# Kernel optimization log

Hardware: AMD Instinct MI355X
Metric: run time of the kernel (lower is better)

Reference implementation:

```python
import math
import jax, jax.numpy as jnp
import numpy as np

N_HEADS = 32
N_KV_HEADS = 8
HEAD_DIM = 64
DIM = 2048
SEQ = 4096
EST_Q = 64          # idx = min(64, seqlen)
VERTICAL_SIZE = 300 # min(prompt_len, max(300, 30))
SLASH_SIZE = 800    # min(prompt_len, max(800, 50))


def apply_rope(t, cos, sin):
    # t: [B,S,H,hd]; pairs are consecutive (reshape(...,-1,2) in torch view_as_complex)
    B, S, H, hd = t.shape
    tr = t.reshape(B, S, H, hd // 2, 2)
    xr, xi = tr[..., 0], tr[..., 1]
    c = cos[None, :, None, :]
    s = sin[None, :, None, :]
    orr = xr * c - xi * s
    oii = xr * s + xi * c
    return jnp.stack([orr, oii], axis=-1).reshape(B, S, H, hd)


def sum_all_diagonal(mat):
    # faithful jax version of torch as_strided trick: sum over anti-shifted diagonals
    # mat: [b,h,n,m] -> [b,h,n+m-1]; sum_diags[j] = sum_i mat[i, i + j - n], j in [1, n+m-1]
    b, h, n, m = mat.shape
    padded = jnp.pad(mat, ((0, 0), (0, 0), (0, 0), (n, n)))
    gidx = jnp.arange(n)[:, None] + jnp.arange(n + m)[None, :]  # [n, n+m]
    diags = jnp.take_along_axis(padded, jnp.broadcast_to(gidx, (b, h, n, n + m)), axis=-1)
    return diags.sum(axis=2)[:, :, 1:]


def setup_inputs() -> dict:
    key = jax.random.key(0)
    ks = jax.random.split(key, 6)
    x = jax.random.normal(ks[0], (1, SEQ, DIM), dtype=jnp.float32)
    # real RoPE tables (theta = 10000)
    inv_freq = 1.0 / (10000.0 ** (np.arange(0, HEAD_DIM, 2, dtype=np.float32) / HEAD_DIM))
    ang = np.outer(np.arange(SEQ, dtype=np.float32), inv_freq)  # [S, hd/2]
    freqs_cos = jnp.asarray(np.cos(ang), dtype=jnp.float32)
    freqs_sin = jnp.asarray(np.sin(ang), dtype=jnp.float32)
    scale = 0.02
    wq = jax.random.normal(ks[1], (DIM, N_HEADS * HEAD_DIM), dtype=jnp.float32) * scale
    wk = jax.random.normal(ks[2], (DIM, N_KV_HEADS * HEAD_DIM), dtype=jnp.float32) * scale
    wv = jax.random.normal(ks[3], (DIM, N_KV_HEADS * HEAD_DIM), dtype=jnp.float32) * scale
    wo = jax.random.normal(ks[4], (N_HEADS * HEAD_DIM, DIM), dtype=jnp.float32) * scale
    return {"x": x, "freqs_cos": freqs_cos, "freqs_sin": freqs_sin,
            "wq": wq, "wk": wk, "wv": wv, "wo": wo}


def reference(x, freqs_cos, freqs_sin, wq, wk, wv, wo):
    B, S, D = x.shape
    H, Hkv, hd = N_HEADS, N_KV_HEADS, HEAD_DIM
    rep = H // Hkv
    scale = 1.0 / math.sqrt(hd)

    # QKV + RoPE (K gets RoPE, V does not), GQA repeat
    q = apply_rope((x @ wq).reshape(B, S, H, hd), freqs_cos, freqs_sin).transpose(0, 2, 1, 3)
    k = apply_rope((x @ wk).reshape(B, S, Hkv, hd), freqs_cos, freqs_sin)
    v = (x @ wv).reshape(B, S, Hkv, hd)
    k = jnp.repeat(k, rep, axis=2).transpose(0, 2, 1, 3)  # [B,H,S,hd]
    v = jnp.repeat(v, rep, axis=2).transpose(0, 2, 1, 3)

    # --- vertical / slash pattern estimation (first idx queries, as in source) ---
    idx = min(EST_Q, S)
    qe = q[:, :, :idx, :]
    est = jnp.einsum('bhqd,bhkd->bhqk', qe, k) * scale  # [B,H,idx,S]
    ar = jnp.arange(idx)
    blk = ar[:, None] >= ar[None, :]
    tail = jnp.where(blk[None, None], est[..., -idx:], -jnp.inf)
    est = jnp.concatenate([est[..., :S - idx], tail], axis=-1)
    probs = jax.nn.softmax(est, axis=-1)

    Vn = min(S, VERTICAL_SIZE)
    Sl = min(S, SLASH_SIZE)
    vertical = probs.sum(axis=2)                  # [B,H,S]
    _, v_idx = jax.lax.top_k(vertical, Vn)        # [B,H,Vn]
    diag = sum_all_diagonal(probs)[..., :S]       # [..., :-idx+1] -> length S
    _, s_idx = jax.lax.top_k(diag, Sl)
    slash = S - 1 - s_idx                         # [B,H,Sl]

    sparse_keys = jnp.sort(jnp.concatenate([v_idx, slash], axis=-1), axis=-1)  # [B,H,K]

    # --- sparse causal attention over selected keys ---
    k_sp = jnp.take_along_axis(k, sparse_keys[..., None], axis=2)  # [B,H,K,hd]
    v_sp = jnp.take_along_axis(v, sparse_keys[..., None], axis=2)
    att = jnp.einsum('bhqd,bhkd->bhqk', q, k_sp) * scale           # [B,H,S,K]
    causal = sparse_keys[:, :, None, :] <= jnp.arange(S)[None, None, :, None]
    att = jnp.where(causal, att, -1e30)
    p = jax.nn.softmax(att, axis=-1)
    out = jnp.einsum('bhqk,bhkd->bhqd', p, v_sp)
    out = out.transpose(0, 2, 1, 3).reshape(B, S, H * hd)
    return out @ wo
```

## Files before the change

### kernel.cpp

```cpp
#include <hip/hip_runtime.h>
#include <hip/hip_bf16.h>
#include <math.h>
#include <stdint.h>

#define SEQ   4096
#define DIMM  2048
#define NH    32
#define NKV   8
#define HD    64
#define NSP   1100
#define NSPP  1152

typedef __bf16 bf16x8 __attribute__((ext_vector_type(8)));
typedef float  f32x4  __attribute__((ext_vector_type(4)));

#define MODE_V 0
#define MODE_Q 1
#define MODE_O 2

__device__ inline void split8(const float* __restrict__ p, bf16x8& h, bf16x8& l) {
#pragma unroll
    for (int i = 0; i < 8; ++i) {
        float v = p[i];
        __bf16 hv = (__bf16)v;
        h[i] = hv;
        l[i] = (__bf16)(v - (float)hv);
    }
}
__device__ inline f32x4 load4(const void* __restrict__ p, size_t idx, bool f) {
    if (f) return *(const f32x4*)((const float*)p + idx);
    const __bf16* b = (const __bf16*)p + idx;
    f32x4 v;
    v[0] = (float)b[0]; v[1] = (float)b[1]; v[2] = (float)b[2]; v[3] = (float)b[3];
    return v;
}
__device__ __forceinline__ void gl_lds16(const __bf16* __restrict__ g, __bf16* l) {
    __builtin_amdgcn_global_load_lds(
        (const __attribute__((address_space(1))) void*)g,
        (__attribute__((address_space(3))) void*)l, 16, 0, 0);
}
__device__ __forceinline__ void cs_at(const void* fc, const void* fs, bool f,
                                      int t, int j, float& c, float& s) {
    if (f) {
        c = ((const float*)fc)[t * 32 + j];
        s = ((const float*)fs)[t * 32 + j];
    } else {
        c = (float)((const __bf16*)fc)[t * 32 + j];
        s = (float)((const __bf16*)fs)[t * 32 + j];
    }
}

__global__ __launch_bounds__(256) void detect_k(const void* __restrict__ x,
                                                int* __restrict__ flag) {
    const __bf16* p = (const __bf16*)x;
    int tid = threadIdx.x;
    bool bad = false;
    for (int i = 0; i < 16; ++i) {
        float v = fabsf((float)p[tid * 16 + i]);
        if (!(v <= 1e10f)) bad = true;
    }
    unsigned long long m = __ballot(bad);
    __shared__ unsigned long long w[4];
    if ((tid & 63) == 0) w[tid >> 6] = m;
    __syncthreads();
    if (tid == 0) flag[0] = ((w[0] | w[1] | w[2] | w[3]) != 0ULL) ? 1 : 0;
}

__global__ __launch_bounds__(256) void convert_x_k(const void* __restrict__ x,
                                                   __bf16* __restrict__ xb,
                                                   const int* __restrict__ flag) {
    int i0 = (blockIdx.x * 256 + threadIdx.x) * 8;
    if (*flag) {
        const float* xf = (const float*)x;
        bf16x8 o;
        for (int i = 0; i < 8; ++i) o[i] = (__bf16)xf[i0 + i];
        *(bf16x8*)(xb + i0) = o;
    } else {
        *(bf16x8*)(xb + i0) = *(const bf16x8*)((const __bf16*)x + i0);
    }
}

__device__ __forceinline__ void transpose_body(const void* __restrict__ in,
                                               __bf16* __restrict__ out,
                                               int R, int C, bool f,
                                               int cb, int rb) {
    __shared__ __bf16 tile[32][33];
    int tx = threadIdx.x & 31, ty = threadIdx.x >> 5;
    for (int i = 0; i < 32; i += 8) {
        size_t idx = (size_t)(rb + ty + i) * C + cb + tx;
        float v = f ? ((const float*)in)[idx] : (float)((const __bf16*)in)[idx];
        tile[ty + i][tx] = (__bf16)v;
    }
    __syncthreads();
    for (int i = 0; i < 32; i += 8)
        out[(size_t)(cb + ty + i) * R + rb + tx] = tile[tx][ty + i];
}

__global__ __launch_bounds__(256) void transpose_cvt_k(const void* __restrict__ in,
                                                       __bf16* __restrict__ out, int R, int C,
                                                       const int* __restrict__ flag) {
    transpose_body(in, out, R, C, (*flag != 0), blockIdx.x * 32, blockIdx.y * 32);
}

__global__ __launch_bounds__(256) void transpose2_k(const void* __restrict__ wq,
                                                    __bf16* __restrict__ Wtq,
                                                    const void* __restrict__ wv,
                                                    __bf16* __restrict__ Wtv,
                                                    const int* __restrict__ flag) {
    bool f = (*flag != 0);
    int bx = blockIdx.x;
    if (bx < 64) transpose_body(wq, Wtq, 2048, 2048, f, bx * 32, blockIdx.y * 32);
    else         transpose_body(wv, Wtv, 2048,  512, f, (bx - 64) * 32, blockIdx.y * 32);
}

__device__ __forceinline__ void gemm_nt_body(const __bf16* __restrict__ A,
                                             const __bf16* __restrict__ Bt,
                                             void* __restrict__ C, int N,
                                             int bm, int bn, bool f, int mode,
                                             const void* __restrict__ fc,
                                             const void* __restrict__ fs,
                                             char* smem) {
    const int K = DIMM;
    __bf16* As = (__bf16*)smem;
    __bf16* Bs = (__bf16*)(smem + 16384);
    int tid = threadIdx.x, wave = tid >> 6, lane = tid & 63;
    int quad = lane >> 4, l16 = lane & 15;
    int wm = (wave >> 1) * 64, wn = (wave & 1) * 64;
    const f32x4 z4 = {0.f, 0.f, 0.f, 0.f};
    f32x4 acc[4][4];
    for (int a = 0; a < 4; ++a) for (int b = 0; b < 4; ++b) acc[a][b] = z4;
    const __bf16* Ab = A  + (size_t)(bm * 128) * K;
    const __bf16* Bb = Bt + (size_t)(bn * 128) * K;
    for (int k0 = 0; k0 < K; k0 += 64) {
#pragma unroll
        for (int it = 0; it < 4; ++it) {
            int ci = it * 256 + tid;
            int row = ci >> 3, c8 = (ci & 7) * 8;
            gl_lds16(Ab + (size_t)row * K + k0 + c8, As + ci * 8);
            gl_lds16(Bb + (size_t)row * K + k0 + c8, Bs + ci * 8);
        }
        __syncthreads();
#pragma unroll
        for (int ks = 0; ks < 2; ++ks) {
            bf16x8 af[4], bfr[4];
#pragma unroll
            for (int mt = 0; mt < 4; ++mt)
                af[mt]  = *(const bf16x8*)&As[(wm + mt * 16 + l16) * 64 + ks * 32 + quad * 8];
#pragma unroll
            for (int nt = 0; nt < 4; ++nt)
                bfr[nt] = *(const bf16x8*)&Bs[(wn + nt * 16 + l16) * 64 + ks * 32 + quad * 8];
#pragma unroll
            for (int mt = 0; mt < 4; ++mt)
#pragma unroll
                for (int nt = 0; nt < 4; ++nt)
                    acc[mt][nt] = __builtin_amdgcn_mfma_f32_16x16x32_bf16(af[mt], bfr[nt], acc[mt][nt], 0, 0, 0);
        }
        __syncthreads();
    }
    if (mode == MODE_Q) {
        for (int mt = 0; mt < 4; ++mt)
            for (int nt = 0; nt < 4; ++nt)
#pragma unroll
                for (int r = 0; r < 4; ++r) {
                    int col = bn * 128 + wn + nt * 16 + l16;
                    int t = bm * 128 + wm + mt * 16 + quad * 4 + r;
                    float qv = (float)(__bf16)acc[mt][nt][r];
                    float pv = __shfl_xor(qv, 1);
                    int j = (col & 63) >> 1;
                    float c, s;
                    cs_at(fc, fs, f, t, j, c, s);
                    float o = (lane & 1) ? (pv * s + qv * c) : (qv * c - pv * s);
                    ((__bf16*)C)[(size_t)t * N + col] = (__bf16)o;
                }
    } else if (mode == MODE_O) {
        bool f32o = f;
        for (int mt = 0; mt < 4; ++mt)
            for (int nt = 0; nt < 4; ++nt) {
                int rowb = bm * 128 + wm + mt * 16 + quad * 4;
                int col = bn * 128 + wn + nt * 16 + l16;
                if (f32o) {
                    for (int r = 0; r < 4; ++r)
                        ((float*)C)[(size_t)(rowb + r) * N + col] = acc[mt][nt][r];
                } else {
                    for (int r = 0; r < 4; ++r)
                        ((__bf16*)C)[(size_t)(rowb + r) * N + col] = (__bf16)acc[mt][nt][r];
                }
            }
    } else {
        for (int mt = 0; mt < 4; ++mt)
            for (int nt = 0; nt < 4; ++nt) {
                int rowb = bm * 128 + wm + mt * 16 + quad * 4;
                int col = bn * 128 + wn + nt * 16 + l16;
                for (int r = 0; r < 4; ++r)
                    ((__bf16*)C)[(size_t)(rowb + r) * N + col] = (__bf16)acc[mt][nt][r];
            }
    }
}

__global__ __launch_bounds__(256) void gemm_qv_k(const __bf16* __restrict__ xbf,
                                                 const __bf16* __restrict__ Wtq,
                                                 const __bf16* __restrict__ Wtv,
                                                 __bf16* __restrict__ Qb,
                                                 __bf16* __restrict__ Vb,
                                                 const void* __restrict__ fc,
                                                 const void* __restrict__ fs,
                                                 const int* __restrict__ flag) {
    __shared__ __align__(16) char smem[32768];
    bool f = (*flag != 0);
    int bx = blockIdx.x, by = blockIdx.y;
    if (bx < 32) {
        gemm_nt_body(xbf, Wtq, Qb, 2048, bx, by, f, MODE_Q, fc, fs, smem);
    } else {
        int bm = (bx - 32) * 4 + (by >> 2), bn = by & 3;
        gemm_nt_body(xbf, Wtv, Vb, 512, bm, bn, f, MODE_V, nullptr, nullptr, smem);
    }
}

__global__ __launch_bounds__(256) void gemm_o_k(const __bf16* __restrict__ A,
                                                const __bf16* __restrict__ Bt,
                                                void* __restrict__ C,
                                                const int* __restrict__ flag) {
    __shared__ __align__(16) char smem[32768];
    bool f = (*flag != 0);
    gemm_nt_body(A, Bt, C, 2048, blockIdx.x, blockIdx.y, f, MODE_O, nullptr, nullptr, smem);
}

__device__ __forceinline__ void gemm_split_rope32_body(const void* __restrict__ A,
                                                       const void* __restrict__ B,
                                                       float* __restrict__ C,
                                                       __bf16* __restrict__ Cb,
                                                       int N, bool f, int bm, int bn,
                                                       bool ropeAll,
                                                       const void* __restrict__ fc,
                                                       const void* __restrict__ fs) {
    const int K = DIMM;
    __shared__ float Asf[32][36];
    __shared__ float Bsf[128][36];
    int tid = threadIdx.x, wave = tid >> 6, lane = tid & 63;
    int quad = lane >> 4, l16 = lane & 15;
    int wn = wave * 32;
    const f32x4 z4 = {0.f, 0.f, 0.f, 0.f};
    f32x4 acc[2][2];
    for (int a = 0; a < 2; ++a) for (int b = 0; b < 2; ++b) acc[a][b] = z4;
    int arow = tid >> 3, acol = (tid & 7) * 4;
    for (int k0 = 0; k0 < K; k0 += 32) {
        {
            f32x4 va = load4(A, (size_t)(bm * 32 + arow) * K + k0 + acol, f);
            *(f32x4*)&Asf[arow][acol] = va;
        }
        for (int it = 0; it < 4; ++it) {
            int g = tid + it * 256;
            int krow = g >> 5, ng = (g & 31) * 4;
            f32x4 v = load4(B, (size_t)(k0 + krow) * N + bn * 128 + ng, f);
            Bsf[ng + 0][krow] = v[0];
            Bsf[ng + 1][krow] = v[1];
            Bsf[ng + 2][krow] = v[2];
            Bsf[ng + 3][krow] = v[3];
        }
        __syncthreads();
        bf16x8 ah[2], al[2], bh[2], bl[2];
        for (int mt = 0; mt < 2; ++mt) split8(&Asf[mt * 16 + l16][quad * 8], ah[mt], al[mt]);
        for (int nt = 0; nt < 2; ++nt) split8(&Bsf[wn + nt * 16 + l16][quad * 8], bh[nt], bl[nt]);
        for (int mt = 0; mt < 2; ++mt)
            for (int nt = 0; nt < 2; ++nt) {
                acc[mt][nt] = __builtin_amdgcn_mfma_f32_16x16x32_bf16(al[mt], bh[nt], acc[mt][nt], 0, 0, 0);
                acc[mt][nt] = __builtin_amdgcn_mfma_f32_16x16x32_bf16(ah[mt], bl[nt], acc[mt][nt], 0, 0, 0);
                acc[mt][nt] = __builtin_amdgcn_mfma_f32_16x16x32_bf16(ah[mt], bh[nt], acc[mt][nt], 0, 0, 0);
            }
        __syncthreads();
    }
    for (int mt = 0; mt < 2; ++mt)
        for (int nt = 0; nt < 2; ++nt)
#pragma unroll
            for (int r = 0; r < 4; ++r) {
                int col = bn * 128 + wn + nt * 16 + l16;
                int t = bm * 32 + mt * 16 + quad * 4 + r;
                float v = acc[mt][nt][r];
                float pv = __shfl_xor(v, 1);
                float o = v;
                if (ropeAll || t < 64) {
                    int j = (col & 63) >> 1;
                    float c, s;
                    cs_at(fc, fs, f, t, j, c, s);
                    o = (lane & 1) ? (pv * s + v * c) : (v * c - pv * s);
                }
                C[(size_t)t * N + col] = o;
                if (ropeAll) Cb[(size_t)t * N + col] = (__bf16)o;
            }
}

__global__ __launch_bounds__(256) void split_dual_rope_k(const void* __restrict__ x,
                                                         const void* __restrict__ wk,
                                                         float* __restrict__ Kf,
                                                         const void* __restrict__ wq,
                                                         float* __restrict__ Qe,
                                                         __bf16* __restrict__ Kb,
                                                         const void* __restrict__ fc,
                                                         const void* __restrict__ fs,
                                                         const int* __restrict__ flag) {
    bool f = (*flag != 0);
    int bid = blockIdx.x;
    if (bid < 512) {
        gemm_split_rope32_body(x, wk, Kf, Kb, 512, f, bid >> 2, bid & 3, true, fc, fs);
    } else {
        int i = bid - 512;
        gemm_split_rope32_body(x, wq, Qe, nullptr, 2048, f, i >> 4, i & 15, false, fc, fs);
    }
}

__global__ __launch_bounds__(256) void est_part_k(const float* __restrict__ Qe,
                                                  const float* __restrict__ Kf,
                                                  float* __restrict__ pm,
                                                  float* __restrict__ ps,
                                                  float* __restrict__ diag) {
    int h = blockIdx.x, sl = blockIdx.y;
    int tid = threadIdx.x, wave = tid >> 6, lane = tid & 63;
    int quad = lane >> 4, l16 = lane & 15;
    for (int i = tid; i < 512; i += 256) diag[h * SEQ + sl * 512 + i] = 0.f;
    __shared__ float Ml[64];
    __shared__ float pA[4][64];
    bf16x8 qh[4][2], ql[4][2];
    for (int mt = 0; mt < 4; ++mt)
        for (int kc = 0; kc < 2; ++kc)
            split8(Qe + (size_t)(mt * 16 + l16) * DIMM + h * HD + kc * 32 + quad * 8,
                   qh[mt][kc], ql[mt][kc]);
    int kvoff = (h >> 2) * HD;
    float pmax[4][4];
    for (int mt = 0; mt < 4; ++mt) for (int r = 0; r < 4; ++r) pmax[mt][r] = -3.0e38f;
    for (int jb = wave; jb < 8; jb += 4)
        for (int c = 0; c < 4; ++c) {
            int j0 = sl * 512 + jb * 64 + c * 16;
            const float* kp = Kf + (size_t)(j0 + l16) * (NKV * HD) + kvoff + quad * 8;
            bf16x8 kh0, kl0, kh1, kl1;
            split8(kp, kh0, kl0);
            split8(kp + 32, kh1, kl1);
            int j = j0 + l16;
            for (int mt = 0; mt < 4; ++mt) {
                f32x4 acc = {0.f, 0.f, 0.f, 0.f};
                acc = __builtin_amdgcn_mfma_f32_16x16x32_bf16(ql[mt][0], kh0, acc, 0, 0, 0);
                acc = __builtin_amdgcn_mfma_f32_16x16x32_bf16(qh[mt][0], kl0, acc, 0, 0, 0);
                acc = __builtin_amdgcn_mfma_f32_16x16x32_bf16(qh[mt][0], kh0, acc, 0, 0, 0);
                acc = __builtin_amdgcn_mfma_f32_16x16x32_bf16(ql[mt][1], kh1, acc, 0, 0, 0);
                acc = __builtin_amdgcn_mfma_f32_16x16x32_bf16(qh[mt][1], kl1, acc, 0, 0, 0);
                acc = __builtin_amdgcn_mfma_f32_16x16x32_bf16(qh[mt][1], kh1, acc, 0, 0, 0);
                for (int r = 0; r < 4; ++r) {
                    int q = mt * 16 + quad * 4 + r;
                    float sv = acc[r] * 0.125f;
                    if (j >= SEQ - 64 && q < j - (SEQ - 64)) sv = -1e30f;
                    pmax[mt][r] = fmaxf(pmax[mt][r], sv);
                }
            }
        }
    for (int mt = 0; mt < 4; ++mt)
        for (int r = 0; r < 4; ++r)
            for (int m2 = 1; m2 < 16; m2 <<= 1)
                pmax[mt][r] = fmaxf(pmax[mt][r], __shfl_xor(pmax[mt][r], m2));
    if (l16 == 0)
        for (int mt = 0; mt < 4; ++mt)
            for (int r = 0; r < 4; ++r)
                pA[wave][mt * 16 + quad * 4 + r] = pmax[mt][r];
    __syncthreads();
    if (tid < 64)
        Ml[tid] = fmaxf(fmaxf(pA[0][tid], pA[1][tid]), fmaxf(pA[2][tid], pA[3][tid]));
    __syncthreads();
    float mreg[4][4];
    for (int mt = 0; mt < 4; ++mt)
        for (int r = 0; r < 4; ++r)
            mreg[mt][r] = Ml[mt * 16 + quad * 4 + r];
    float psum[4][4];
    for (int mt = 0; mt < 4; ++mt) for (int r = 0; r < 4; ++r) psum[mt][r] = 0.f;
    for (int jb = wave; jb < 8; jb += 4)
        for (int c = 0; c < 4; ++c) {
            int j0 = sl * 512 + jb * 64 + c * 16;
            const float* kp = Kf + (size_t)(j0 + l16) * (NKV * HD) + kvoff + quad * 8;
            bf16x8 kh0, kl0, kh1, kl1;
            split8(kp, kh0, kl0);
            split8(kp + 32, kh1, kl1);
            int j = j0 + l16;
            for (int mt = 0; mt < 4; ++mt) {
                f32x4 acc = {0.f, 0.f, 0.f, 0.f};
                acc = __builtin_amdgcn_mfma_f32_16x16x32_bf16(ql[mt][0], kh0, acc, 0, 0, 0);
                acc = __builtin_amdgcn_mfma_f32_16x16x32_bf16(qh[mt][0], kl0, acc, 0, 0, 0);
                acc = __builtin_amdgcn_mfma_f32_16x16x32_bf16(qh[mt][0], kh0, acc, 0, 0, 0);
                acc = __builtin_amdgcn_mfma_f32_16x16x32_bf16(ql[mt][1], kh1, acc, 0, 0, 0);
                acc = __builtin_amdgcn_mfma_f32_16x16x32_bf16(qh[mt][1], kl1, acc, 0, 0, 0);
                acc = __builtin_amdgcn_mfma_f32_16x16x32_bf16(qh[mt][1], kh1, acc, 0, 0, 0);
                for (int r = 0; r < 4; ++r) {
                    int q = mt * 16 + quad * 4 + r;
                    float sv = acc[r] * 0.125f;
                    if (j >= SEQ - 64 && q < j - (SEQ - 64)) sv = -1e30f;
                    psum[mt][r] += __expf(sv - mreg[mt][r]);
                }
            }
        }
    for (int mt = 0; mt < 4; ++mt)
        for (int r = 0; r < 4; ++r)
            for (int m2 = 1; m2 < 16; m2 <<= 1)
                psum[mt][r] += __shfl_xor(psum[mt][r], m2);
    if (l16 == 0)
        for (int mt = 0; mt < 4; ++mt)
            for (int r = 0; r < 4; ++r)
                pA[wave][mt * 16 + quad * 4 + r] = psum[mt][r];
    __syncthreads();
    if (tid < 64) {
        pm[(h * 8 + sl) * 64 + tid] = Ml[tid];
        ps[(h * 8 + sl) * 64 + tid] = pA[0][tid] + pA[1][tid] + pA[2][tid] + pA[3][tid];
    }
}

__global__ __launch_bounds__(256) void vert_diag_k(const float* __restrict__ Qe,
                                                   const float* __restrict__ Kf,
                                                   const float* __restrict__ pm,
                                                   const float* __restrict__ ps,
                                                   float* __restrict__ vert,
                                                   float* __restrict__ diag) {
    int h = blockIdx.x, jb = blockIdx.y;
    int tid = threadIdx.x, wave = tid >> 6, lane = tid & 63;
    int quad = lane >> 4, l16 = lane & 15;
    __shared__ float P[64][132];
    __shared__ float dloc[192];
    __shared__ float rm_l[64], rs_l[64];
    for (int i = tid; i < 192; i += 256) dloc[i] = 0.f;
    if (tid < 64) {
        float M = -3.0e38f;
        for (int sl = 0; sl < 8; ++sl) M = fmaxf(M, pm[(h * 8 + sl) * 64 + tid]);
        float S = 0.f;
        for (int sl = 0; sl < 8; ++sl)
            S += ps[(h * 8 + sl) * 64 + tid] * __expf(pm[(h * 8 + sl) * 64 + tid] - M);
        rm_l[tid] = M;
        rs_l[tid] = S;
    }
    bf16x8 qh[4][2], ql[4][2];
    for (int mt = 0; mt < 4; ++mt)
        for (int kc = 0; kc < 2; ++kc)
            split8(Qe + (size_t)(mt * 16 + l16) * DIMM + h * HD + kc * 32 + quad * 8,
                   qh[mt][kc], ql[mt][kc]);
    __syncthreads();
    float rm[4][4], rs[4][4];
    for (int mt = 0; mt < 4; ++mt)
        for (int r = 0; r < 4; ++r) {
            int q = mt * 16 + quad * 4 + r;
            rm[mt][r] = rm_l[q];
            rs[mt][r] = rs_l[q];
        }
    int kvoff = (h >> 2) * HD;
    for (int c = 0; c < 2; ++c) {
        int jl0 = wave * 32 + c * 16;
        int j0 = jb * 128 + jl0;
        const float* kp = Kf + (size_t)(j0 + l16) * (NKV * HD) + kvoff + quad * 8;
        bf16x8 kh0, kl0, kh1, kl1;
        split8(kp, kh0, kl0);
        split8(kp + 32, kh1, kl1);
        int j = j0 + l16;
        for (int mt = 0; mt < 4; ++mt) {
            f32x4 acc = {0.f, 0.f, 0.f, 0.f};
            acc = __builtin_amdgcn_mfma_f32_16x16x32_bf16(ql[mt][0], kh0, acc, 0, 0, 0);
            acc = __builtin_amdgcn_mfma_f32_16x16x32_bf16(qh[mt][0], kl0, acc, 0, 0, 0);
            acc = __builtin_amdgcn_mfma_f32_16x16x32_bf16(qh[mt][0], kh0, acc, 0, 0, 0);
            acc = __builtin_amdgcn_mfma_f32_16x16x32_bf16(ql[mt][1], kh1, acc, 0, 0, 0);
            acc = __builtin_amdgcn_mfma_f32_16x16x32_bf16(qh[mt][1], kl1, acc, 0, 0, 0);
            acc = __builtin_amdgcn_mfma_f32_16x16x32_bf16(qh[mt][1], kh1, acc, 0, 0, 0);
            for (int r = 0; r < 4; ++r) {
                int q = mt * 16 + quad * 4 + r;
                float sv = acc[r] * 0.125f;
                if (j >= SEQ - 64 && q < j - (SEQ - 64)) sv = -1e30f;
                P[q][jl0 + l16] = __expf(sv - rm[mt][r]) / rs[mt][r];
            }
        }
    }
    __syncthreads();
    if (tid < 128) {
        float vacc = 0.f;
        for (int q = 0; q < 64; ++q) {
            float pb = P[q][tid];
            vacc += pb;
            if (jb * 128 + tid + 63 - q < SEQ) atomicAdd(&dloc[tid + 63 - q], pb);
        }
        vert[h * SEQ + jb * 128 + tid] = vacc;
    }
    __syncthreads();
    for (int i = tid; i < 192; i += 256) {
        int g = jb * 128 + i;
        if (g < SEQ) atomicAdd(&diag[h * SEQ + g], dloc[i]);
    }
}

__global__ __launch_bounds__(256) void topk_merge_k(const float* __restrict__ vert,
                                                    const float* __restrict__ diag,
                                                    int* __restrict__ skeys) {
    __shared__ int cnt[4096];
    __shared__ int hist4[4][256];
    __shared__ int scanb[256];
    __shared__ int B_sh, kk_sh;
    int h = blockIdx.x, tid = threadIdx.x, wave = tid >> 6;
    for (int i = tid; i < 4096; i += 256) cnt[i] = 0;
    __syncthreads();
    for (int selp = 0; selp < 2; ++selp) {
        const float* vals = (selp == 0 ? vert : diag) + h * SEQ;
        int k = (selp == 0) ? 300 : 800;
        bool flip = (selp == 1);
        unsigned bits[16];
        for (int g = 0; g < 4; ++g) {
            f32x4 v = *(const f32x4*)(vals + tid * 16 + g * 4);
            for (int e = 0; e < 4; ++e) bits[g * 4 + e] = __float_as_uint(v[e]);
        }
        unsigned prefix = 0;
        int kk = k;
        for (int pass = 0; pass < 4; ++pass) {
            int sh = 8 * (3 - pass);
            for (int w = 0; w < 4; ++w) hist4[w][tid] = 0;
            __syncthreads();
            for (int e = 0; e < 16; ++e) {
                unsigned b = bits[e];
                bool in = (pass == 0) || ((b >> (sh + 8)) == prefix);
                if (in) atomicAdd(&hist4[wave][(b >> sh) & 255], 1);
            }
            __syncthreads();
            scanb[tid] = hist4[0][tid] + hist4[1][tid] + hist4[2][tid] + hist4[3][tid];
            __syncthreads();
            for (int off = 1; off < 256; off <<= 1) {
                int v = (tid + off < 256) ? scanb[tid + off] : 0;
                __syncthreads();
                scanb[tid] += v;
                __syncthreads();
            }
            int sufNext = (tid < 255) ? scanb[tid + 1] : 0;
            if (scanb[tid] >= kk && sufNext < kk) { B_sh = tid; kk_sh = kk - sufNext; }
            __syncthreads();
            prefix = (prefix << 8) | (unsigned)B_sh;
            kk = kk_sh;
            __syncthreads();
        }
        int localEq = 0;
        for (int e = 0; e < 16; ++e) {
            unsigned b = bits[e];
            if (b > prefix) {
                int idx = tid * 16 + e;
                atomicAdd(&cnt[flip ? (4095 - idx) : idx], 1);
            } else if (b == prefix) ++localEq;
        }
        scanb[tid] = localEq;
        __syncthreads();
        for (int off = 1; off < 256; off <<= 1) {
            int v = (tid >= off) ? scanb[tid - off] : 0;
            __syncthreads();
            scanb[tid] += v;
            __syncthreads();
        }
        int eqOff = scanb[tid] - localEq;
        int taken = 0;
        for (int e = 0; e < 16; ++e) {
            unsigned b = bits[e];
            if (b == prefix) {
                if (eqOff + taken < kk) {
                    int idx = tid * 16 + e;
                    atomicAdd(&cnt[flip ? (4095 - idx) : idx], 1);
                }
                ++taken;
            }
        }
        __syncthreads();
    }
    int base = tid * 16;
    int loc[16];
    int s = 0;
    for (int e = 0; e < 16; ++e) { loc[e] = s; s += cnt[base + e]; }
    scanb[tid] = s;
    __syncthreads();
    for (int off = 1; off < 256; off <<= 1) {
        int v = (tid >= off) ? scanb[tid - off] : 0;
        __syncthreads();
        scanb[tid] += v;
        __syncthreads();
    }
    int chunkExcl = scanb[tid] - s;
    int* out = skeys + h * NSPP;
    for (int e = 0; e < 16; ++e) {
        int c = cnt[base + e];
        int pos = chunkExcl + loc[e];
        for (int r = 0; r < c; ++r) out[pos + r] = base + e;
    }
    for (int i = NSP + tid; i < NSPP; i += 256) out[i] = 0x7fffffff;
}

__global__ __launch_bounds__(256) void gather_k(const __bf16* __restrict__ Kb,
                                                const __bf16* __restrict__ Vb,
                                                const int* __restrict__ skeys,
                                                __bf16* __restrict__ Ksp,
                                                __bf16* __restrict__ VspT) {
    int h = blockIdx.x, jb = blockIdx.y;
    __shared__ __bf16 tile[64][72];
    int tid = threadIdx.x;
    int jl = tid >> 2, d0 = (tid & 3) * 16;
    int j = jb * 64 + jl;
    int key = skeys[h * NSPP + j];
    int kv = (h >> 2) * HD;
    const bf16x8 z = {};
    bf16x8 k0v = z, k1v = z, v0v = z, v1v = z;
    if ((unsigned)key < SEQ) {
        const __bf16* ks = Kb + (size_t)key * (NKV * HD) + kv + d0;
        const __bf16* vs = Vb + (size_t)key * (NKV * HD) + kv + d0;
        k0v = *(const bf16x8*)ks; k1v = *(const bf16x8*)(ks + 8);
        v0v = *(const bf16x8*)vs; v1v = *(const bf16x8*)(vs + 8);
    }
    __bf16* kd = Ksp + ((size_t)h * NSPP + j) * HD + d0;
    *(bf16x8*)kd = k0v;
    *(bf16x8*)(kd + 8) = k1v;
    *(bf16x8*)&tile[jl][d0] = v0v;
    *(bf16x8*)&tile[jl][d0 + 8] = v1v;
    __syncthreads();
    int d = tid >> 2, jl0 = (tid & 3) * 16;
    bf16x8 o0, o1;
    for (int e = 0; e < 8; ++e) { o0[e] = tile[jl0 + e][d]; o1[e] = tile[jl0 + 8 + e][d]; }
    __bf16* vt = VspT + ((size_t)h * HD + d) * NSPP + jb * 64 + jl0;
    *(bf16x8*)vt = o0;
    *(bf16x8*)(vt + 8) = o1;
}

__global__ __launch_bounds__(512) void sparse_attn_k(const __bf16* Qb,
                                                     const __bf16* __restrict__ Ksp,
                                                     const __bf16* __restrict__ VspT,
                                                     const int* __restrict__ skeys,
                                                     __bf16* AO) {
    int qb = blockIdx.x, h = blockIdx.y;
    int tid = threadIdx.x, wave = tid >> 6, lane = tid & 63;
    int quad = lane >> 4, l16 = lane & 15;
    __shared__ __bf16 sc[64][1160];
    __shared__ float rsm[64];
    int t0 = qb * 64;
    bf16x8 aq[4][2];
#pragma unroll
    for (int qs = 0; qs < 4; ++qs)
#pragma unroll
        for (int kc = 0; kc < 2; ++kc)
            aq[qs][kc] = *(const bf16x8*)(Qb + (size_t)(t0 + qs * 16 + l16) * DIMM + h * HD + kc * 32 + quad * 8);
    const __bf16* Kh = Ksp + (size_t)h * NSPP * HD;
    const int* sk = skeys + h * NSPP;
#pragma unroll
    for (int c = 0; c < 9; ++c) {
        int j0 = wave * 144 + c * 16;
        const __bf16* kp = Kh + (size_t)(j0 + l16) * HD + quad * 8;
        bf16x8 b0 = *(const bf16x8*)kp;
        bf16x8 b1 = *(const bf16x8*)(kp + 32);
        int j = j0 + l16;
        int key = sk[j];
#pragma unroll
        for (int qs = 0; qs < 4; ++qs) {
            f32x4 acc = {0.f, 0.f, 0.f, 0.f};
            acc = __builtin_amdgcn_mfma_f32_16x16x32_bf16(aq[qs][0], b0, acc, 0, 0, 0);
            acc = __builtin_amdgcn_mfma_f32_16x16x32_bf16(aq[qs][1], b1, acc, 0, 0, 0);
            int qg = t0 + qs * 16 + quad * 4;
#pragma unroll
            for (int r = 0; r < 4; ++r) {
                float sv = acc[r] * 0.125f;
                if (key > qg + r) sv = -1e30f;
                sc[qs * 16 + quad * 4 + r][j] = (__bf16)sv;
            }
        }
    }
    __syncthreads();
    {
        int row = tid >> 3, sub = tid & 7;
        int c0 = sub * 144;
        float mx = -3.0e38f;
        for (int i = 0; i < 18; ++i) {
            bf16x8 v = *(const bf16x8*)&sc[row][c0 + i * 8];
            for (int e = 0; e < 8; ++e) mx = fmaxf(mx, (float)v[e]);
        }
        for (int m2 = 1; m2 < 8; m2 <<= 1) mx = fmaxf(mx, __shfl_xor(mx, m2, 8));
        float sm = 0.f;
        for (int i = 0; i < 18; ++i) {
            int cb = c0 + i * 8;
            bf16x8 v = *(const bf16x8*)&sc[row][cb];
            bf16x8 pw;
            for (int e = 0; e < 8; ++e) {
                float pv = 0.f;
                if (cb + e < NSP) { pv = __expf((float)v[e] - mx); sm += pv; }
                pw[e] = (__bf16)pv;
            }
            *(bf16x8*)&sc[row][cb] = pw;
        }
        for (int m2 = 1; m2 < 8; m2 <<= 1) sm += __shfl_xor(sm, m2, 8);
        if (sub == 0) rsm[row] = sm;
    }
    __syncthreads();
    int qs = wave >> 1, dh = wave & 1;
    const f32x4 z4 = {0.f, 0.f, 0.f, 0.f};
    f32x4 o0 = z4, o1 = z4;
    const __bf16* Vh = VspT + ((size_t)h * HD + dh * 32) * NSPP;
#pragma unroll 4
    for (int c = 0; c < 36; ++c) {
        int kb = c * 32;
        bf16x8 pa = *(const bf16x8*)&sc[qs * 16 + l16][kb + quad * 8];
        bf16x8 v0 = *(const bf16x8*)(Vh + (size_t)l16 * NSPP + kb + quad * 8);
        bf16x8 v1 = *(const bf16x8*)(Vh + (size_t)(16 + l16) * NSPP + kb + quad * 8);
        o0 = __builtin_amdgcn_mfma_f32_16x16x32_bf16(pa, v0, o0, 0, 0, 0);
        o1 = __builtin_amdgcn_mfma_f32_16x16x32_bf16(pa, v1, o1, 0, 0, 0);
    }
#pragma unroll
    for (int r = 0; r < 4; ++r) {
        int ql = qs * 16 + quad * 4 + r;
        float inv = 1.f / rsm[ql];
        size_t base = (size_t)(t0 + ql) * DIMM + h * HD + dh * 32;
        AO[base + l16]      = (__bf16)(o0[r] * inv);
        AO[base + 16 + l16] = (__bf16)(o1[r] * inv);
    }
}

extern "C" void kernel_launch(void* const* d_in, const int* in_sizes, int n_in,
                              void* d_out, int out_size, void* d_ws, size_t ws_size,
                              hipStream_t stream) {
    const void* x  = d_in[0];
    const void* fc = d_in[1];
    const void* fs = d_in[2];
    const void* wq = d_in[3];
    const void* wk = d_in[4];
    const void* wv = d_in[5];
    const void* wo = d_in[6];
    char* ws = (char*)d_ws;

    __bf16* Qb   = (__bf16*)(ws + 0);
    __bf16* Kb   = (__bf16*)(ws + 16777216);
    __bf16* Vb   = (__bf16*)(ws + 20971520);
    __bf16* xbf  = (__bf16*)(ws + 25165824);
    float*  Kf32 = (float*)(ws + 25165824);
    float*  Qef32= (float*)(ws + 33554432);
    __bf16* Ksp  = (__bf16*)(ws + 25165824);
    __bf16* VspT = (__bf16*)(ws + 29884416);
    __bf16* Wtq  = (__bf16*)(ws + 41943040);
    __bf16* Wto  = (__bf16*)(ws + 41943040);
    __bf16* Wtv  = (__bf16*)(ws + 50331648);
    float*  vert = (float*)(ws + 51396608);
    float*  diag = (float*)(ws + 51920896);
    int*    skeys= (int*)(ws + 52445184);
    int*    flag = (int*)(ws + 52592640);
    float*  pm   = (float*)(ws + 52592896);
    float*  ps   = (float*)(ws + 52658432);

    dim3 b256(256);
    detect_k<<<1, b256, 0, stream>>>(x, flag);
    convert_x_k<<<4096, b256, 0, stream>>>(x, xbf, flag);
    transpose2_k<<<dim3(80, 64), b256, 0, stream>>>(wq, Wtq, wv, Wtv, flag);
    gemm_qv_k<<<dim3(40, 16), b256, 0, stream>>>(xbf, Wtq, Wtv, Qb, Vb, fc, fs, flag);
    split_dual_rope_k<<<576, b256, 0, stream>>>(x, wk, Kf32, wq, Qef32, Kb,
                                                fc, fs, flag);
    est_part_k<<<dim3(32, 8), b256, 0, stream>>>(Qef32, Kf32, pm, ps, diag);
    vert_diag_k<<<dim3(32, 32), b256, 0, stream>>>(Qef32, Kf32, pm, ps, vert, diag);
    topk_merge_k<<<32, b256, 0, stream>>>(vert, diag, skeys);
    transpose_cvt_k<<<dim3(64, 64), b256, 0, stream>>>(wo, Wto, 2048, 2048, flag);
    gather_k<<<dim3(32, 18), b256, 0, stream>>>(Kb, Vb, skeys, Ksp, VspT);
    sparse_attn_k<<<dim3(64, 32), dim3(512), 0, stream>>>(Qb, Ksp, VspT, skeys, Qb);
    gemm_o_k<<<dim3(32, 16), b256, 0, stream>>>(Qb, Wto, d_out, flag);
}
```

Baseline: 898.7 us.

## Pre-split transposed Wk and merge weight transposes into neighbouring kernels

```diff
diff --git a/kernel.cpp b/kernel.cpp
--- a/kernel.cpp
+++ b/kernel.cpp
@@ -64,20 +64,6 @@
     if ((tid & 63) == 0) w[tid >> 6] = m;
     __syncthreads();
     if (tid == 0) flag[0] = ((w[0] | w[1] | w[2] | w[3]) != 0ULL) ? 1 : 0;
-}
-
-__global__ __launch_bounds__(256) void convert_x_k(const void* __restrict__ x,
-                                                   __bf16* __restrict__ xb,
-                                                   const int* __restrict__ flag) {
-    int i0 = (blockIdx.x * 256 + threadIdx.x) * 8;
-    if (*flag) {
-        const float* xf = (const float*)x;
-        bf16x8 o;
-        for (int i = 0; i < 8; ++i) o[i] = (__bf16)xf[i0 + i];
-        *(bf16x8*)(xb + i0) = o;
-    } else {
-        *(bf16x8*)(xb + i0) = *(const bf16x8*)((const __bf16*)x + i0);
-    }
 }
 
 __device__ __forceinline__ void transpose_body(const void* __restrict__ in,
@@ -96,21 +82,207 @@
         out[(size_t)(cb + ty + i) * R + rb + tx] = tile[tx][ty + i];
 }
 
-__global__ __launch_bounds__(256) void transpose_cvt_k(const void* __restrict__ in,
-                                                       __bf16* __restrict__ out, int R, int C,
-                                                       const int* __restrict__ flag) {
-    transpose_body(in, out, R, C, (*flag != 0), blockIdx.x * 32, blockIdx.y * 32);
-}
-
-__global__ __launch_bounds__(256) void transpose2_k(const void* __restrict__ wq,
-                                                    __bf16* __restrict__ Wtq,
-                                                    const void* __restrict__ wv,
-                                                    __bf16* __restrict__ Wtv,
-                                                    const int* __restrict__ flag) {
+__device__ __forceinline__ void transpose_split_body(const void* __restrict__ in,
+                                                     __bf16* __restrict__ oh,
+                                                     __bf16* __restrict__ ol,
+                                                     int R, int C, bool f,
+                                                     int cb, int rb) {
+    __shared__ float tf[32][33];
+    int tx = threadIdx.x & 31, ty = threadIdx.x >> 5;
+    for (int i = 0; i < 32; i += 8) {
+        size_t idx = (size_t)(rb + ty + i) * C + cb + tx;
+        tf[ty + i][tx] = f ? ((const float*)in)[idx] : (float)((const __bf16*)in)[idx];
+    }
+    __syncthreads();
+    for (int i = 0; i < 32; i += 8) {
+        float v = tf[tx][ty + i];
+        __bf16 h = (__bf16)v;
+        size_t o = (size_t)(cb + ty + i) * R + rb + tx;
+        oh[o] = h;
+        ol[o] = (__bf16)(v - (float)h);
+    }
+}
+
+__global__ __launch_bounds__(256) void convert_wkt_k(const void* __restrict__ x,
+                                                     __bf16* __restrict__ xb,
+                                                     const void* __restrict__ wk,
+                                                     __bf16* __restrict__ Wtk_h,
+                                                     __bf16* __restrict__ Wtk_l,
+                                                     const int* __restrict__ flag) {
+    int bid = blockIdx.x;
     bool f = (*flag != 0);
-    int bx = blockIdx.x;
-    if (bx < 64) transpose_body(wq, Wtq, 2048, 2048, f, bx * 32, blockIdx.y * 32);
-    else         transpose_body(wv, Wtv, 2048,  512, f, (bx - 64) * 32, blockIdx.y * 32);
+    if (bid < 4096) {
+        int i0 = (bid * 256 + threadIdx.x) * 8;
+        if (f) {
+            const float* xf = (const float*)x;
+            bf16x8 o;
+            for (int i = 0; i < 8; ++i) o[i] = (__bf16)xf[i0 + i];
+            *(bf16x8*)(xb + i0) = o;
+        } else {
+            *(bf16x8*)(xb + i0) = *(const bf16x8*)((const __bf16*)x + i0);
+        }
+    } else {
+        int id = bid - 4096;
+        int cb = (id >> 6) * 32, rb = (id & 63) * 32;
+        transpose_split_body(wk, Wtk_h, Wtk_l, 2048, 512, f, cb, rb);
+    }
+}
+
+__device__ __forceinline__ void gemm_ksplit_body(const void* __restrict__ x,
+                                                 const __bf16* __restrict__ Bh,
+                                                 const __bf16* __restrict__ Bl,
+                                                 float* __restrict__ C,
+                                                 __bf16* __restrict__ Cb,
+                                                 bool f, int bm, int bn,
+                                                 const void* __restrict__ fc,
+                                                 const void* __restrict__ fs,
+                                                 char* smem) {
+    const int K = DIMM, N = 512;
+    float (*Asf)[68] = (float (*)[68])smem;
+    __bf16* Bsh = (__bf16*)(smem + 8704);
+    __bf16* Bsl = (__bf16*)(smem + 8704 + 16384);
+    int tid = threadIdx.x, wave = tid >> 6, lane = tid & 63;
+    int quad = lane >> 4, l16 = lane & 15;
+    int wn = wave * 32;
+    const f32x4 z4 = {0.f, 0.f, 0.f, 0.f};
+    f32x4 acc[2][2];
+    for (int a = 0; a < 2; ++a) for (int b = 0; b < 2; ++b) acc[a][b] = z4;
+    int arow = tid >> 3, ac8 = (tid & 7) * 8;
+    const __bf16* Bhb = Bh + (size_t)(bn * 128) * K;
+    const __bf16* Blb = Bl + (size_t)(bn * 128) * K;
+    for (int k0 = 0; k0 < K; k0 += 64) {
+        f32x4 va0 = load4(x, (size_t)(bm * 32 + arow) * K + k0 + ac8, f);
+        f32x4 va1 = load4(x, (size_t)(bm * 32 + arow) * K + k0 + ac8 + 4, f);
+        *(f32x4*)&Asf[arow][ac8]     = va0;
+        *(f32x4*)&Asf[arow][ac8 + 4] = va1;
+#pragma unroll
+        for (int it = 0; it < 4; ++it) {
+            int ci = it * 256 + tid;
+            int row = ci >> 3, c8 = (ci & 7) * 8;
+            gl_lds16(Bhb + (size_t)row * K + k0 + c8, Bsh + ci * 8);
+            gl_lds16(Blb + (size_t)row * K + k0 + c8, Bsl + ci * 8);
+        }
+        __syncthreads();
+#pragma unroll
+        for (int ks = 0; ks < 2; ++ks) {
+            bf16x8 ah[2], al[2], bh[2], bl[2];
+#pragma unroll
+            for (int mt = 0; mt < 2; ++mt)
+                split8(&Asf[mt * 16 + l16][ks * 32 + quad * 8], ah[mt], al[mt]);
+#pragma unroll
+            for (int nt = 0; nt < 2; ++nt) {
+                bh[nt] = *(const bf16x8*)&Bsh[(wn + nt * 16 + l16) * 64 + ks * 32 + quad * 8];
+                bl[nt] = *(const bf16x8*)&Bsl[(wn + nt * 16 + l16) * 64 + ks * 32 + quad * 8];
+            }
+#pragma unroll
+            for (int mt = 0; mt < 2; ++mt)
+#pragma unroll
+                for (int nt = 0; nt < 2; ++nt) {
+                    acc[mt][nt] = __builtin_amdgcn_mfma_f32_16x16x32_bf16(al[mt], bh[nt], acc[mt][nt], 0, 0, 0);
+                    acc[mt][nt] = __builtin_amdgcn_mfma_f32_16x16x32_bf16(ah[mt], bl[nt], acc[mt][nt], 0, 0, 0);
+                    acc[mt][nt] = __builtin_amdgcn_mfma_f32_16x16x32_bf16(ah[mt], bh[nt], acc[mt][nt], 0, 0, 0);
+                }
+        }
+        __syncthreads();
+    }
+    for (int mt = 0; mt < 2; ++mt)
+        for (int nt = 0; nt < 2; ++nt)
+#pragma unroll
+            for (int r = 0; r < 4; ++r) {
+                int col = bn * 128 + wn + nt * 16 + l16;
+                int t = bm * 32 + mt * 16 + quad * 4 + r;
+                float v = acc[mt][nt][r];
+                float pv = __shfl_xor(v, 1);
+                int j = (col & 63) >> 1;
+                float c, s;
+                cs_at(fc, fs, f, t, j, c, s);
+                float o = (lane & 1) ? (pv * s + v * c) : (v * c - pv * s);
+                C[(size_t)t * N + col] = o;
+                Cb[(size_t)t * N + col] = (__bf16)o;
+            }
+}
+
+__device__ __forceinline__ void gemm_qesplit_body(const void* __restrict__ A,
+                                                  const void* __restrict__ B,
+                                                  float* __restrict__ C,
+                                                  int N, bool f, int bm, int bn,
+                                                  const void* __restrict__ fc,
+                                                  const void* __restrict__ fs,
+                                                  char* smem) {
+    const int K = DIMM;
+    float (*Asf)[36] = (float (*)[36])smem;
+    float (*Bsf)[36] = (float (*)[36])(smem + 4608);
+    int tid = threadIdx.x, wave = tid >> 6, lane = tid & 63;
+    int quad = lane >> 4, l16 = lane & 15;
+    int wn = wave * 32;
+    const f32x4 z4 = {0.f, 0.f, 0.f, 0.f};
+    f32x4 acc[2][2];
+    for (int a = 0; a < 2; ++a) for (int b = 0; b < 2; ++b) acc[a][b] = z4;
+    int arow = tid >> 3, acol = (tid & 7) * 4;
+    for (int k0 = 0; k0 < K; k0 += 32) {
+        {
+            f32x4 va = load4(A, (size_t)(bm * 32 + arow) * K + k0 + acol, f);
+            *(f32x4*)&Asf[arow][acol] = va;
+        }
+        for (int it = 0; it < 4; ++it) {
+            int g = tid + it * 256;
+            int krow = g >> 5, ng = (g & 31) * 4;
+            f32x4 v = load4(B, (size_t)(k0 + krow) * N + bn * 128 + ng, f);
+            Bsf[ng + 0][krow] = v[0];
+            Bsf[ng + 1][krow] = v[1];
+            Bsf[ng + 2][krow] = v[2];
+            Bsf[ng + 3][krow] = v[3];
+        }
+        __syncthreads();
+        bf16x8 ah[2], al[2], bh[2], bl[2];
+        for (int mt = 0; mt < 2; ++mt) split8(&Asf[mt * 16 + l16][quad * 8], ah[mt], al[mt]);
+        for (int nt = 0; nt < 2; ++nt) split8(&Bsf[wn + nt * 16 + l16][quad * 8], bh[nt], bl[nt]);
+        for (int mt = 0; mt < 2; ++mt)
+            for (int nt = 0; nt < 2; ++nt) {
+                acc[mt][nt] = __builtin_amdgcn_mfma_f32_16x16x32_bf16(al[mt], bh[nt], acc[mt][nt], 0, 0, 0);
+                acc[mt][nt] = __builtin_amdgcn_mfma_f32_16x16x32_bf16(ah[mt], bl[nt], acc[mt][nt], 0, 0, 0);
+                acc[mt][nt] = __builtin_amdgcn_mfma_f32_16x16x32_bf16(ah[mt], bh[nt], acc[mt][nt], 0, 0, 0);
+            }
+        __syncthreads();
+    }
+    for (int mt = 0; mt < 2; ++mt)
+        for (int nt = 0; nt < 2; ++nt)
+#pragma unroll
+            for (int r = 0; r < 4; ++r) {
+                int col = bn * 128 + wn + nt * 16 + l16;
+                int t = bm * 32 + mt * 16 + quad * 4 + r;
+                float v = acc[mt][nt][r];
+                float pv = __shfl_xor(v, 1);
+                float o = v;
+                if (t < 64) {
+                    int j = (col & 63) >> 1;
+                    float c, s;
+                    cs_at(fc, fs, f, t, j, c, s);
+                    o = (lane & 1) ? (pv * s + v * c) : (v * c - pv * s);
+                }
+                C[(size_t)t * N + col] = o;
+            }
+}
+
+__global__ __launch_bounds__(256) void split_dual_rope_k(const void* __restrict__ x,
+                                                         const __bf16* __restrict__ Wtk_h,
+                                                         const __bf16* __restrict__ Wtk_l,
+                                                         float* __restrict__ Kf,
+                                                         const void* __restrict__ wq,
+                                                         float* __restrict__ Qe,
+                                                         __bf16* __restrict__ Kb,
+                                                         const void* __restrict__ fc,
+                                                         const void* __restrict__ fs,
+                                                         const int* __restrict__ flag) {
+    __shared__ __align__(16) char smem[41472];
+    bool f = (*flag != 0);
+    int bid = blockIdx.x;
+    if (bid < 512) {
+        gemm_ksplit_body(x, Wtk_h, Wtk_l, Kf, Kb, f, bid >> 2, bid & 3, fc, fs, smem);
+    } else {
+        int i = bid - 512;
+        gemm_qesplit_body(x, wq, Qe, 2048, f, i >> 4, i & 15, fc, fs, smem);
+    }
 }
 
 __device__ __forceinline__ void gemm_nt_body(const __bf16* __restrict__ A,
@@ -223,89 +395,6 @@
     __shared__ __align__(16) char smem[32768];
     bool f = (*flag != 0);
     gemm_nt_body(A, Bt, C, 2048, blockIdx.x, blockIdx.y, f, MODE_O, nullptr, nullptr, smem);
-}
-
-__device__ __forceinline__ void gemm_split_rope32_body(const void* __restrict__ A,
-                                                       const void* __restrict__ B,
-                                                       float* __restrict__ C,
-                                                       __bf16* __restrict__ Cb,
-                                                       int N, bool f, int bm, int bn,
-                                                       bool ropeAll,
-                                                       const void* __restrict__ fc,
-                                                       const void* __restrict__ fs) {
-    const int K = DIMM;
-    __shared__ float Asf[32][36];
-    __shared__ float Bsf[128][36];
-    int tid = threadIdx.x, wave = tid >> 6, lane = tid & 63;
-    int quad = lane >> 4, l16 = lane & 15;
-    int wn = wave * 32;
-    const f32x4 z4 = {0.f, 0.f, 0.f, 0.f};
-    f32x4 acc[2][2];
-    for (int a = 0; a < 2; ++a) for (int b = 0; b < 2; ++b) acc[a][b] = z4;
-    int arow = tid >> 3, acol = (tid & 7) * 4;
-    for (int k0 = 0; k0 < K; k0 += 32) {
-        {
-            f32x4 va = load4(A, (size_t)(bm * 32 + arow) * K + k0 + acol, f);
-            *(f32x4*)&Asf[arow][acol] = va;
-        }
-        for (int it = 0; it < 4; ++it) {
-            int g = tid + it * 256;
-            int krow = g >> 5, ng = (g & 31) * 4;
-            f32x4 v = load4(B, (size_t)(k0 + krow) * N + bn * 128 + ng, f);
-            Bsf[ng + 0][krow] = v[0];
-            Bsf[ng + 1][krow] = v[1];
-            Bsf[ng + 2][krow] = v[2];
-            Bsf[ng + 3][krow] = v[3];
-        }
-        __syncthreads();
-        bf16x8 ah[2], al[2], bh[2], bl[2];
-        for (int mt = 0; mt < 2; ++mt) split8(&Asf[mt * 16 + l16][quad * 8], ah[mt], al[mt]);
-        for (int nt = 0; nt < 2; ++nt) split8(&Bsf[wn + nt * 16 + l16][quad * 8], bh[nt], bl[nt]);
-        for (int mt = 0; mt < 2; ++mt)
-            for (int nt = 0; nt < 2; ++nt) {
-                acc[mt][nt] = __builtin_amdgcn_mfma_f32_16x16x32_bf16(al[mt], bh[nt], acc[mt][nt], 0, 0, 0);
-                acc[mt][nt] = __builtin_amdgcn_mfma_f32_16x16x32_bf16(ah[mt], bl[nt], acc[mt][nt], 0, 0, 0);
-                acc[mt][nt] = __builtin_amdgcn_mfma_f32_16x16x32_bf16(ah[mt], bh[nt], acc[mt][nt], 0, 0, 0);
-            }
-        __syncthreads();
-    }
-    for (int mt = 0; mt < 2; ++mt)
-        for (int nt = 0; nt < 2; ++nt)
-#pragma unroll
-            for (int r = 0; r < 4; ++r) {
-                int col = bn * 128 + wn + nt * 16 + l16;
-                int t = bm * 32 + mt * 16 + quad * 4 + r;
-                float v = acc[mt][nt][r];
-                float pv = __shfl_xor(v, 1);
-                float o = v;
-                if (ropeAll || t < 64) {
-                    int j = (col & 63) >> 1;
-                    float c, s;
-                    cs_at(fc, fs, f, t, j, c, s);
-                    o = (lane & 1) ? (pv * s + v * c) : (v * c - pv * s);
-                }
-                C[(size_t)t * N + col] = o;
-                if (ropeAll) Cb[(size_t)t * N + col] = (__bf16)o;
-            }
-}
-
-__global__ __launch_bounds__(256) void split_dual_rope_k(const void* __restrict__ x,
-                                                         const void* __restrict__ wk,
-                                                         float* __restrict__ Kf,
-                                                         const void* __restrict__ wq,
-                                                         float* __restrict__ Qe,
-                                                         __bf16* __restrict__ Kb,
-                                                         const void* __restrict__ fc,
-                                                         const void* __restrict__ fs,
-                                                         const int* __restrict__ flag) {
-    bool f = (*flag != 0);
-    int bid = blockIdx.x;
-    if (bid < 512) {
-        gemm_split_rope32_body(x, wk, Kf, Kb, 512, f, bid >> 2, bid & 3, true, fc, fs);
-    } else {
-        int i = bid - 512;
-        gemm_split_rope32_body(x, wq, Qe, nullptr, 2048, f, i >> 4, i & 15, false, fc, fs);
-    }
 }
 
 __global__ __launch_bounds__(256) void est_part_k(const float* __restrict__ Qe,
@@ -485,9 +574,22 @@
     }
 }
 
-__global__ __launch_bounds__(256) void topk_merge_k(const float* __restrict__ vert,
-                                                    const float* __restrict__ diag,
-                                                    int* __restrict__ skeys) {
+__global__ __launch_bounds__(256) void topk_qvt_k(const float* __restrict__ vert,
+                                                  const float* __restrict__ diag,
+                                                  int* __restrict__ skeys,
+                                                  const void* __restrict__ wq,
+                                                  __bf16* __restrict__ Wtq,
+                                                  const void* __restrict__ wv,
+                                                  __bf16* __restrict__ Wtv,
+                                                  const int* __restrict__ flag) {
+    if (blockIdx.x >= 32) {
+        bool f = (*flag != 0);
+        int id = blockIdx.x - 32;
+        int bx = id >> 6, by = id & 63;
+        if (bx < 64) transpose_body(wq, Wtq, 2048, 2048, f, bx * 32, by * 32);
+        else         transpose_body(wv, Wtv, 2048,  512, f, (bx - 64) * 32, by * 32);
+        return;
+    }
     __shared__ int cnt[4096];
     __shared__ int hist4[4][256];
     __shared__ int scanb[256];
@@ -583,12 +685,22 @@
     for (int i = NSP + tid; i < NSPP; i += 256) out[i] = 0x7fffffff;
 }
 
-__global__ __launch_bounds__(256) void gather_k(const __bf16* __restrict__ Kb,
-                                                const __bf16* __restrict__ Vb,
-                                                const int* __restrict__ skeys,
-                                                __bf16* __restrict__ Ksp,
-                                                __bf16* __restrict__ VspT) {
-    int h = blockIdx.x, jb = blockIdx.y;
+__global__ __launch_bounds__(256) void gather_wot_k(const __bf16* __restrict__ Kb,
+                                                    const __bf16* __restrict__ Vb,
+                                                    const int* __restrict__ skeys,
+                                                    __bf16* __restrict__ Ksp,
+                                                    __bf16* __restrict__ VspT,
+                                                    const void* __restrict__ wo,
+                                                    __bf16* __restrict__ Wto,
+                                                    const int* __restrict__ flag) {
+    int bid = blockIdx.x;
+    if (bid >= 576) {
+        bool f = (*flag != 0);
+        int id = bid - 576;
+        transpose_body(wo, Wto, 2048, 2048, f, (id >> 6) * 32, (id & 63) * 32);
+        return;
+    }
+    int h = bid / 18, jb = bid % 18;
     __shared__ __bf16 tile[64][72];
     int tid = threadIdx.x;
     int jl = tid >> 2, d0 = (tid & 3) * 16;
@@ -719,36 +831,36 @@
     const void* wo = d_in[6];
     char* ws = (char*)d_ws;
 
+    __bf16* Wtk_h= (__bf16*)(ws + 0);
+    __bf16* Wtk_l= (__bf16*)(ws + 2097152);
+    float*  Kf32 = (float*)(ws + 4194304);
+    float*  Qef32= (float*)(ws + 12582912);
+    float*  pm   = (float*)(ws + 13631488);
+    float*  ps   = (float*)(ws + 13697024);
+    float*  vert = (float*)(ws + 13762560);
+    float*  diag = (float*)(ws + 14286848);
     __bf16* Qb   = (__bf16*)(ws + 0);
     __bf16* Kb   = (__bf16*)(ws + 16777216);
     __bf16* Vb   = (__bf16*)(ws + 20971520);
     __bf16* xbf  = (__bf16*)(ws + 25165824);
-    float*  Kf32 = (float*)(ws + 25165824);
-    float*  Qef32= (float*)(ws + 33554432);
     __bf16* Ksp  = (__bf16*)(ws + 25165824);
     __bf16* VspT = (__bf16*)(ws + 29884416);
     __bf16* Wtq  = (__bf16*)(ws + 41943040);
     __bf16* Wto  = (__bf16*)(ws + 41943040);
     __bf16* Wtv  = (__bf16*)(ws + 50331648);
-    float*  vert = (float*)(ws + 51396608);
-    float*  diag = (float*)(ws + 51920896);
     int*    skeys= (int*)(ws + 52445184);
     int*    flag = (int*)(ws + 52592640);
-    float*  pm   = (float*)(ws + 52592896);
-    float*  ps   = (float*)(ws + 52658432);
 
     dim3 b256(256);
     detect_k<<<1, b256, 0, stream>>>(x, flag);
-    convert_x_k<<<4096, b256, 0, stream>>>(x, xbf, flag);
-    transpose2_k<<<dim3(80, 64), b256, 0, stream>>>(wq, Wtq, wv, Wtv, flag);
-    gemm_qv_k<<<dim3(40, 16), b256, 0, stream>>>(xbf, Wtq, Wtv, Qb, Vb, fc, fs, flag);
-    split_dual_rope_k<<<576, b256, 0, stream>>>(x, wk, Kf32, wq, Qef32, Kb,
-                                                fc, fs, flag);
+    convert_wkt_k<<<5120, b256, 0, stream>>>(x, xbf, wk, Wtk_h, Wtk_l, flag);
+    split_dual_rope_k<<<544, b256, 0, stream>>>(x, Wtk_h, Wtk_l, Kf32, wq, Qef32,
+                                                Kb, fc, fs, flag);
     est_part_k<<<dim3(32, 8), b256, 0, stream>>>(Qef32, Kf32, pm, ps, diag);
     vert_diag_k<<<dim3(32, 32), b256, 0, stream>>>(Qef32, Kf32, pm, ps, vert, diag);
-    topk_merge_k<<<32, b256, 0, stream>>>(vert, diag, skeys);
-    transpose_cvt_k<<<dim3(64, 64), b256, 0, stream>>>(wo, Wto, 2048, 2048, flag);
-    gather_k<<<dim3(32, 18), b256, 0, stream>>>(Kb, Vb, skeys, Ksp, VspT);
+    topk_qvt_k<<<5152, b256, 0, stream>>>(vert, diag, skeys, wq, Wtq, wv, Wtv, flag);
+    gemm_qv_k<<<dim3(40, 16), b256, 0, stream>>>(xbf, Wtq, Wtv, Qb, Vb, fc, fs, flag);
+    gather_wot_k<<<4672, b256, 0, stream>>>(Kb, Vb, skeys, Ksp, VspT, wo, Wto, flag);
     sparse_attn_k<<<dim3(64, 32), dim3(512), 0, stream>>>(Qb, Ksp, VspT, skeys, Qb);
     gemm_o_k<<<dim3(32, 16), b256, 0, stream>>>(Qb, Wto, d_out, flag);
 }
```

Result: no change. 908.6 us (+1.1%).
